# Kernel optimization log

Measured on AMD Instinct MI355X. Metric: run time of the kernel, lower is better.

Reference implementation:

```python
import jax, jax.numpy as jnp
import numpy as np

IN_DIM = 128
NUM_IDX = 128
LATENT = 512
FF_HID = 4 * IN_DIM
EPS = 1e-5


def _layernorm(x, g, b):
    mu = jnp.mean(x, axis=-1, keepdims=True)
    var = jnp.mean((x - mu) ** 2, axis=-1, keepdims=True)
    return (x - mu) * jax.lax.rsqrt(var + EPS) * g + b


def setup_inputs() -> dict:
    key = jax.random.key(0)
    ks = jax.random.split(key, 12)
    B, N, D, L = 16, NUM_IDX, IN_DIM, LATENT
    s = lambda fan_in: 1.0 / np.sqrt(fan_in)
    return {
        "in_obs": jax.random.normal(ks[0], (B, N, D), jnp.float32),
        "Wq_w": jax.random.normal(ks[1], (D, L), jnp.float32) * s(D),
        "Wq_b": jax.random.normal(ks[2], (L,), jnp.float32) * s(D),
        "Wk_w": jax.random.normal(ks[3], (D, L), jnp.float32) * s(D),
        "Wk_b": jax.random.normal(ks[4], (L,), jnp.float32) * s(D),
        "wv_w": jax.random.normal(ks[5], (2 * L + 2 * N,), jnp.float32) * s(2 * L + 2 * N),
        "wv_b": jax.random.normal(ks[6], (), jnp.float32) * s(2 * L + 2 * N),
        "g1": jnp.ones((D,), jnp.float32),
        "b1": jnp.zeros((D,), jnp.float32),
        "ff1_w": jax.random.normal(ks[7], (D, FF_HID), jnp.float32) * s(D),
        "ff1_b": jax.random.normal(ks[8], (FF_HID,), jnp.float32) * s(D),
        "ff2_w": jax.random.normal(ks[9], (FF_HID, D), jnp.float32) * s(FF_HID),
        "ff2_b": jax.random.normal(ks[10], (D,), jnp.float32) * s(FF_HID),
        "g2": jnp.ones((D,), jnp.float32),
        "b2": jnp.zeros((D,), jnp.float32),
    }


def reference(in_obs, Wq_w, Wq_b, Wk_w, Wk_b, wv_w, wv_b, g1, b1,
              ff1_w, ff1_b, ff2_w, ff2_b, g2, b2):
    # in_obs: [B, N, D]
    B, N, D = in_obs.shape
    L = Wq_w.shape[1]
    eye = jnp.broadcast_to(jnp.eye(N, dtype=in_obs.dtype), (B, N, N))
    # q_cat/k_cat: [B, N, L+N]
    q_cat = jnp.concatenate([in_obs @ Wq_w + Wq_b, eye], axis=-1)
    k_cat = jnp.concatenate([in_obs @ Wk_w + Wk_b, eye], axis=-1)
    # Original: w_v(tanh(concat(q_i, k_j))). tanh is elementwise and the dot
    # product splits over the concat, so score[b,i,j] = a[b,i] + c[b,j] + bias
    # -- mathematically identical, avoids the [B,N,N,2L+2N] intermediate.
    a = jnp.tanh(q_cat) @ wv_w[: L + N]          # [B, N]
    c = jnp.tanh(k_cat) @ wv_w[L + N:]           # [B, N]
    scores = a[:, :, None] + c[:, None, :] + wv_b  # [B, N, N]
    weights = jax.nn.softmax(scores, axis=-1)
    attn = weights @ in_obs                       # [B, N, D]
    res = _layernorm(attn + in_obs, g1, b1)
    ff = jax.nn.relu(res @ ff1_w + ff1_b) @ ff2_w + ff2_b
    return _layernorm(ff + in_obs, g2, b2)
```

## Files before the change

### kernel.cpp

```cpp
#include <hip/hip_runtime.h>

#define NN 128
#define DD 128
#define LL 512
#define FFH 512
#define TANH1 0.76159415595576489f

typedef __attribute__((ext_vector_type(8))) short bf16x8;
typedef __attribute__((ext_vector_type(4))) float f32x4;

struct alignas(16) f4arr { float v[4]; };

__device__ __forceinline__ unsigned short f2bf(float f) {
    union { float f; unsigned u; } v; v.f = f;
    return (unsigned short)((v.u + 0x7FFFu + ((v.u >> 16) & 1u)) >> 16);
}

__global__ __launch_bounds__(256) void kA(
    const float* __restrict__ in_obs,
    const float* __restrict__ Wk_w,
    const float* __restrict__ Wk_b,
    const float* __restrict__ wv_w,
    const float* __restrict__ ff1_w,
    const float* __restrict__ ff2_w,
    float* __restrict__ c_out,
    unsigned short* __restrict__ W1f,
    unsigned short* __restrict__ W2f)
{
    const int t = threadIdx.x;
    const int wave = t >> 6, lane = t & 63;
    __shared__ float row_lds[8][128];
    __shared__ float red[8][4];

    if (blockIdx.x >= 256) {
        const int bi = blockIdx.x - 256;
        const int l15 = lane & 15, l4 = lane >> 4;
        const int fg = (bi & 31) * 4 + wave;
        unsigned short vals[8];
        unsigned short* dst;
        if (bi < 32) {
            const int ks = fg & 3, mt = fg >> 2;
            #pragma unroll
            for (int j = 0; j < 8; ++j)
                vals[j] = f2bf(ff1_w[(ks * 32 + l4 * 8 + j) * FFH + mt * 16 + l15]);
            dst = W1f;
        } else {
            const int ks = fg & 15, mt = fg >> 4;
            #pragma unroll
            for (int j = 0; j < 8; ++j)
                vals[j] = f2bf(ff2_w[(ks * 32 + l4 * 8 + j) * DD + mt * 16 + l15]);
            dst = W2f;
        }
        uint4 u;
        u.x = (unsigned)vals[0] | ((unsigned)vals[1] << 16);
        u.y = (unsigned)vals[2] | ((unsigned)vals[3] << 16);
        u.z = (unsigned)vals[4] | ((unsigned)vals[5] << 16);
        u.w = (unsigned)vals[6] | ((unsigned)vals[7] << 16);
        *(uint4*)&dst[(fg * 64 + lane) * 8] = u;
        return;
    }

    const int row0 = blockIdx.x * 8;
    const float* src = in_obs + row0 * DD;
    #pragma unroll
    for (int i = 0; i < 4; ++i) {
        int idx = t + i * 256;
        row_lds[idx >> 7][idx & 127] = src[idx];
    }
    __syncthreads();

    const int l0 = t, l1 = t + 256;
    float acc0[8], acc1[8];
    #pragma unroll
    for (int r = 0; r < 8; ++r) { acc0[r] = 0.f; acc1[r] = 0.f; }

    #pragma unroll 4
    for (int d = 0; d < 128; d += 4) {
        f4arr rbuf[8];
        #pragma unroll
        for (int r = 0; r < 8; ++r)
            rbuf[r] = *(const f4arr*)&row_lds[r][d];
        #pragma unroll
        for (int dd = 0; dd < 4; ++dd) {
            const float w0 = Wk_w[(d + dd) * LL + l0];
            const float w1 = Wk_w[(d + dd) * LL + l1];
            #pragma unroll
            for (int r = 0; r < 8; ++r) {
                acc0[r] += rbuf[r].v[dd] * w0;
                acc1[r] += rbuf[r].v[dd] * w1;
            }
        }
    }
    const float kb0 = Wk_b[l0], kb1 = Wk_b[l1];
    const float wv0 = wv_w[640 + l0], wv1 = wv_w[640 + l1];
    float v[8];
    #pragma unroll
    for (int r = 0; r < 8; ++r)
        v[r] = tanhf(acc0[r] + kb0) * wv0 + tanhf(acc1[r] + kb1) * wv1;
    #pragma unroll
    for (int off = 32; off > 0; off >>= 1) {
        #pragma unroll
        for (int r = 0; r < 8; ++r)
            v[r] += __shfl_down(v[r], off, 64);
    }
    if (lane == 0) {
        #pragma unroll
        for (int r = 0; r < 8; ++r) red[r][wave] = v[r];
    }
    __syncthreads();
    if (t < 8) {
        const int row = row0 + t;
        const int j = row & (NN - 1);
        c_out[row] = red[t][0] + red[t][1] + red[t][2] + red[t][3]
                   + TANH1 * wv_w[1152 + j];
    }
}

__global__ __launch_bounds__(512, 4) void kB(
    const float* __restrict__ in_obs,
    const float* __restrict__ c_in,
    const unsigned short* __restrict__ W1f,
    const unsigned short* __restrict__ W2f,
    const float* __restrict__ g1, const float* __restrict__ b1,
    const float* __restrict__ ff1_b,
    const float* __restrict__ ff2_b,
    const float* __restrict__ g2, const float* __restrict__ b2,
    float* __restrict__ out)
{
    const int t = threadIdx.x;
    const int b = blockIdx.x >> 5;
    const int j0 = (blockIdx.x & 31) * 4;
    const int wave = t >> 6, lane = t & 63;
    const int l15 = lane & 15, l4 = lane >> 4;

    __shared__ float part[8][128];
    __shared__ alignas(16) unsigned short res_lds[16 * 128];
    __shared__ alignas(16) unsigned short h_lds[16 * 512];
    __shared__ alignas(16) float o2_lds[16 * 128];

    const float cv0 = c_in[b * NN + lane];
    const float cv1 = c_in[b * NN + lane + 64];
    float mx = fmaxf(cv0, cv1);
    #pragma unroll
    for (int off = 32; off > 0; off >>= 1) mx = fmaxf(mx, __shfl_xor(mx, off, 64));
    float e0 = __expf(cv0 - mx), e1 = __expf(cv1 - mx);
    float sm = e0 + e1;
    #pragma unroll
    for (int off = 32; off > 0; off >>= 1) sm += __shfl_xor(sm, off, 64);
    const float inv = 1.f / sm;
    e0 *= inv; e1 *= inv;

    {
        const float* base = in_obs + (b * NN + wave * 16) * DD;
        float a0 = 0.f, a1 = 0.f;
        #pragma unroll
        for (int jj = 0; jj < 16; ++jj) {
            const int js = wave * 16 + jj;
            const float wj = (wave < 4) ? __shfl(e0, js, 64)
                                        : __shfl(e1, js - 64, 64);
            a0 += wj * base[jj * DD + lane];
            a1 += wj * base[jj * DD + 64 + lane];
        }
        part[wave][lane] = a0;
        part[wave][lane + 64] = a1;
    }
    __syncthreads();

    if (wave < 4) {
        const int r = wave;
        const int row = b * NN + j0 + r;
        const int c0i = lane * 2;
        const float2 xo = *(const float2*)&in_obs[row * DD + c0i];
        float x0 = xo.x, x1 = xo.y;
        #pragma unroll
        for (int g = 0; g < 8; ++g) {
            const float2 p = *(const float2*)&part[g][c0i];
            x0 += p.x; x1 += p.y;
        }
        float s = x0 + x1;
        #pragma unroll
        for (int off = 32; off > 0; off >>= 1) s += __shfl_xor(s, off, 64);
        const float mu = s * (1.f / 128.f);
        const float d0 = x0 - mu, d1 = x1 - mu;
        float vs = d0 * d0 + d1 * d1;
        #pragma unroll
        for (int off = 32; off > 0; off >>= 1) vs += __shfl_xor(vs, off, 64);
        const float rstd = rsqrtf(vs * (1.f / 128.f) + 1e-5f);
        const float2 gv = *(const float2*)&g1[c0i];
        const float2 bv = *(const float2*)&b1[c0i];
        const float r0 = d0 * rstd * gv.x + bv.x;
        const float r1 = d1 * rstd * gv.y + bv.y;
        const unsigned pk = (unsigned)f2bf(r0) | ((unsigned)f2bf(r1) << 16);
        const int swz = (lane * 4) ^ ((r & 7) << 4);
        *(unsigned*)((char*)res_lds + r * 256 + swz) = pk;
    } else {
        #pragma unroll
        for (int k = 0; k < 3; ++k) {
            const int r = wave + k * 4;
            *(unsigned*)((char*)res_lds + r * 256 + lane * 4) = 0u;
        }
    }
    __syncthreads();

    {
        bf16x8 bfrag[4];
        #pragma unroll
        for (int ks = 0; ks < 4; ++ks) {
            const int off = l15 * 256 + ((ks * 64 + l4 * 16) ^ ((l15 & 7) << 4));
            bfrag[ks] = *(const bf16x8*)((const char*)res_lds + off);
        }
        #pragma unroll
        for (int i = 0; i < 4; ++i) {
            const int mt = wave * 4 + i;
            f32x4 acc = {0.f, 0.f, 0.f, 0.f};
            #pragma unroll
            for (int ks = 0; ks < 4; ++ks) {
                const bf16x8 afrag = *(const bf16x8*)(W1f + ((mt * 4 + ks) * 64 + lane) * 8);
                acc = __builtin_amdgcn_mfma_f32_16x16x32_bf16(afrag, bfrag[ks], acc, 0, 0, 0);
            }
            const f4arr bias = *(const f4arr*)&ff1_b[mt * 16 + l4 * 4];
            uint2 pk;
            pk.x = (unsigned)f2bf(fmaxf(acc[0] + bias.v[0], 0.f))
                 | ((unsigned)f2bf(fmaxf(acc[1] + bias.v[1], 0.f)) << 16);
            pk.y = (unsigned)f2bf(fmaxf(acc[2] + bias.v[2], 0.f))
                 | ((unsigned)f2bf(fmaxf(acc[3] + bias.v[3], 0.f)) << 16);
            const int off = l15 * 1024 + ((mt * 32 + l4 * 8) ^ ((l15 & 7) << 4));
            *(uint2*)((char*)h_lds + off) = pk;
        }
    }
    __syncthreads();

    {
        f32x4 acc = {0.f, 0.f, 0.f, 0.f};
        #pragma unroll
        for (int ks = 0; ks < 16; ++ks) {
            const int off = l15 * 1024 + ((ks * 64 + l4 * 16) ^ ((l15 & 7) << 4));
            const bf16x8 bfrag = *(const bf16x8*)((const char*)h_lds + off);
            const bf16x8 afrag = *(const bf16x8*)(W2f + ((wave * 16 + ks) * 64 + lane) * 8);
            acc = __builtin_amdgcn_mfma_f32_16x16x32_bf16(afrag, bfrag, acc, 0, 0, 0);
        }
        const int off = l15 * 512 + ((wave * 64 + l4 * 16) ^ ((l15 & 7) << 4));
        *(f32x4*)((char*)o2_lds + off) = acc;
    }
    __syncthreads();

    if (wave < 4) {
        const int r = wave;
        const int row = b * NN + j0 + r;
        const int c0i = lane * 2;
        const int off = r * 512 + ((lane * 8) ^ ((r & 7) << 4));
        const float2 o2 = *(const float2*)((char*)o2_lds + off);
        const float2 fb = *(const float2*)&ff2_b[c0i];
        const float2 xo = *(const float2*)&in_obs[row * DD + c0i];
        const float f0 = o2.x + fb.x + xo.x;
        const float f1 = o2.y + fb.y + xo.y;
        float s = f0 + f1;
        #pragma unroll
        for (int off2 = 32; off2 > 0; off2 >>= 1) s += __shfl_xor(s, off2, 64);
        const float mu = s * (1.f / 128.f);
        const float d0 = f0 - mu, d1 = f1 - mu;
        float vs = d0 * d0 + d1 * d1;
        #pragma unroll
        for (int off2 = 32; off2 > 0; off2 >>= 1) vs += __shfl_xor(vs, off2, 64);
        const float rstd = rsqrtf(vs * (1.f / 128.f) + 1e-5f);
        const float2 gv = *(const float2*)&g2[c0i];
        const float2 bv = *(const float2*)&b2[c0i];
        float2 o;
        o.x = d0 * rstd * gv.x + bv.x;
        o.y = d1 * rstd * gv.y + bv.y;
        *(float2*)&out[row * DD + c0i] = o;
    }
}

extern "C" void kernel_launch(void* const* d_in, const int* in_sizes, int n_in,
                              void* d_out, int out_size, void* d_ws, size_t ws_size,
                              hipStream_t stream) {
    const float* in_obs = (const float*)d_in[0];
    const float* Wk_w  = (const float*)d_in[3];
    const float* Wk_b  = (const float*)d_in[4];
    const float* wv_w  = (const float*)d_in[5];
    const float* g1    = (const float*)d_in[7];
    const float* b1    = (const float*)d_in[8];
    const float* ff1_w = (const float*)d_in[9];
    const float* ff1_b = (const float*)d_in[10];
    const float* ff2_w = (const float*)d_in[11];
    const float* ff2_b = (const float*)d_in[12];
    const float* g2    = (const float*)d_in[13];
    const float* b2    = (const float*)d_in[14];
    float* outp = (float*)d_out;

    unsigned short* W1f = (unsigned short*)d_ws;
    unsigned short* W2f = W1f + 65536;
    float* c_ws = (float*)((char*)d_ws + 262144);

    kA<<<320, 256, 0, stream>>>(in_obs, Wk_w, Wk_b, wv_w, ff1_w, ff2_w,
                                c_ws, W1f, W2f);
    kB<<<512, 512, 0, stream>>>(in_obs, c_ws, W1f, W2f, g1, b1,
                                ff1_b, ff2_b, g2, b2, outp);
}
```

Measured before the change: 28.17 us.

## Fill all 16 MFMA rows per block in kB and spread weight conversion across more blocks

kB now handles 16 output rows per block instead of 4, so the 16-wide MFMA tile is fully used instead of 12 rows being zero padding. This cuts the grid from 512 to 128 blocks, which removes repeated per-block work: the batch softmax/attention reduction and the full W1f/W2f weight reads. In kA, the bf16 weight-fragment conversion is spread over 256 blocks, each thread packing two values, instead of 64 blocks doing eight values per thread. The trade-off is that 128 kB blocks may leave many CUs idle, and each wave now runs two layernorm rows in sequence.

```diff
diff --git a/kernel.cpp b/kernel.cpp
--- a/kernel.cpp
+++ b/kernel.cpp
@@ -29,37 +29,32 @@
 {
     const int t = threadIdx.x;
     const int wave = t >> 6, lane = t & 63;
-    __shared__ float row_lds[8][128];
-    __shared__ float red[8][4];
 
     if (blockIdx.x >= 256) {
         const int bi = blockIdx.x - 256;
+        const int fg = bi & 127;
+        const int jp = t >> 6;
         const int l15 = lane & 15, l4 = lane >> 4;
-        const int fg = (bi & 31) * 4 + wave;
-        unsigned short vals[8];
+        const int j = jp * 2;
+        unsigned short v0, v1;
         unsigned short* dst;
-        if (bi < 32) {
+        if (bi < 128) {
             const int ks = fg & 3, mt = fg >> 2;
-            #pragma unroll
-            for (int j = 0; j < 8; ++j)
-                vals[j] = f2bf(ff1_w[(ks * 32 + l4 * 8 + j) * FFH + mt * 16 + l15]);
+            v0 = f2bf(ff1_w[(ks * 32 + l4 * 8 + j    ) * FFH + mt * 16 + l15]);
+            v1 = f2bf(ff1_w[(ks * 32 + l4 * 8 + j + 1) * FFH + mt * 16 + l15]);
             dst = W1f;
         } else {
             const int ks = fg & 15, mt = fg >> 4;
-            #pragma unroll
-            for (int j = 0; j < 8; ++j)
-                vals[j] = f2bf(ff2_w[(ks * 32 + l4 * 8 + j) * DD + mt * 16 + l15]);
+            v0 = f2bf(ff2_w[(ks * 32 + l4 * 8 + j    ) * DD + mt * 16 + l15]);
+            v1 = f2bf(ff2_w[(ks * 32 + l4 * 8 + j + 1) * DD + mt * 16 + l15]);
             dst = W2f;
         }
-        uint4 u;
-        u.x = (unsigned)vals[0] | ((unsigned)vals[1] << 16);
-        u.y = (unsigned)vals[2] | ((unsigned)vals[3] << 16);
-        u.z = (unsigned)vals[4] | ((unsigned)vals[5] << 16);
-        u.w = (unsigned)vals[6] | ((unsigned)vals[7] << 16);
-        *(uint4*)&dst[(fg * 64 + lane) * 8] = u;
+        *(unsigned*)&dst[(fg * 64 + lane) * 8 + j] = (unsigned)v0 | ((unsigned)v1 << 16);
         return;
     }
 
+    __shared__ float row_lds[8][128];
+    __shared__ float red[8][4];
     const int row0 = blockIdx.x * 8;
     const float* src = in_obs + row0 * DD;
     #pragma unroll
@@ -128,8 +123,8 @@
     float* __restrict__ out)
 {
     const int t = threadIdx.x;
-    const int b = blockIdx.x >> 5;
-    const int j0 = (blockIdx.x & 31) * 4;
+    const int b = blockIdx.x >> 3;
+    const int j0 = (blockIdx.x & 7) * 16;
     const int wave = t >> 6, lane = t & 63;
     const int l15 = lane & 15, l4 = lane >> 4;
 
@@ -166,38 +161,36 @@
     }
     __syncthreads();
 
-    if (wave < 4) {
-        const int r = wave;
-        const int row = b * NN + j0 + r;
+    {
         const int c0i = lane * 2;
-        const float2 xo = *(const float2*)&in_obs[row * DD + c0i];
-        float x0 = xo.x, x1 = xo.y;
+        float a0 = 0.f, a1 = 0.f;
         #pragma unroll
         for (int g = 0; g < 8; ++g) {
             const float2 p = *(const float2*)&part[g][c0i];
-            x0 += p.x; x1 += p.y;
-        }
-        float s = x0 + x1;
-        #pragma unroll
-        for (int off = 32; off > 0; off >>= 1) s += __shfl_xor(s, off, 64);
-        const float mu = s * (1.f / 128.f);
-        const float d0 = x0 - mu, d1 = x1 - mu;
-        float vs = d0 * d0 + d1 * d1;
-        #pragma unroll
-        for (int off = 32; off > 0; off >>= 1) vs += __shfl_xor(vs, off, 64);
-        const float rstd = rsqrtf(vs * (1.f / 128.f) + 1e-5f);
+            a0 += p.x; a1 += p.y;
+        }
         const float2 gv = *(const float2*)&g1[c0i];
         const float2 bv = *(const float2*)&b1[c0i];
-        const float r0 = d0 * rstd * gv.x + bv.x;
-        const float r1 = d1 * rstd * gv.y + bv.y;
-        const unsigned pk = (unsigned)f2bf(r0) | ((unsigned)f2bf(r1) << 16);
-        const int swz = (lane * 4) ^ ((r & 7) << 4);
-        *(unsigned*)((char*)res_lds + r * 256 + swz) = pk;
-    } else {
-        #pragma unroll
-        for (int k = 0; k < 3; ++k) {
-            const int r = wave + k * 4;
-            *(unsigned*)((char*)res_lds + r * 256 + lane * 4) = 0u;
+        #pragma unroll
+        for (int rr = 0; rr < 2; ++rr) {
+            const int r = wave + rr * 8;
+            const int row = b * NN + j0 + r;
+            const float2 xo = *(const float2*)&in_obs[row * DD + c0i];
+            const float x0 = a0 + xo.x, x1 = a1 + xo.y;
+            float s = x0 + x1;
+            #pragma unroll
+            for (int off = 32; off > 0; off >>= 1) s += __shfl_xor(s, off, 64);
+            const float mu = s * (1.f / 128.f);
+            const float d0 = x0 - mu, d1 = x1 - mu;
+            float vs = d0 * d0 + d1 * d1;
+            #pragma unroll
+            for (int off = 32; off > 0; off >>= 1) vs += __shfl_xor(vs, off, 64);
+            const float rstd = rsqrtf(vs * (1.f / 128.f) + 1e-5f);
+            const float r0 = d0 * rstd * gv.x + bv.x;
+            const float r1 = d1 * rstd * gv.y + bv.y;
+            const unsigned pk = (unsigned)f2bf(r0) | ((unsigned)f2bf(r1) << 16);
+            const int swz = (lane * 4) ^ ((r & 7) << 4);
+            *(unsigned*)((char*)res_lds + r * 256 + swz) = pk;
         }
     }
     __syncthreads();
@@ -244,31 +237,34 @@
     }
     __syncthreads();
 
-    if (wave < 4) {
-        const int r = wave;
-        const int row = b * NN + j0 + r;
+    {
         const int c0i = lane * 2;
-        const int off = r * 512 + ((lane * 8) ^ ((r & 7) << 4));
-        const float2 o2 = *(const float2*)((char*)o2_lds + off);
         const float2 fb = *(const float2*)&ff2_b[c0i];
-        const float2 xo = *(const float2*)&in_obs[row * DD + c0i];
-        const float f0 = o2.x + fb.x + xo.x;
-        const float f1 = o2.y + fb.y + xo.y;
-        float s = f0 + f1;
-        #pragma unroll
-        for (int off2 = 32; off2 > 0; off2 >>= 1) s += __shfl_xor(s, off2, 64);
-        const float mu = s * (1.f / 128.f);
-        const float d0 = f0 - mu, d1 = f1 - mu;
-        float vs = d0 * d0 + d1 * d1;
-        #pragma unroll
-        for (int off2 = 32; off2 > 0; off2 >>= 1) vs += __shfl_xor(vs, off2, 64);
-        const float rstd = rsqrtf(vs * (1.f / 128.f) + 1e-5f);
         const float2 gv = *(const float2*)&g2[c0i];
         const float2 bv = *(const float2*)&b2[c0i];
-        float2 o;
-        o.x = d0 * rstd * gv.x + bv.x;
-        o.y = d1 * rstd * gv.y + bv.y;
-        *(float2*)&out[row * DD + c0i] = o;
+        #pragma unroll
+        for (int rr = 0; rr < 2; ++rr) {
+            const int r = wave + rr * 8;
+            const int row = b * NN + j0 + r;
+            const int off = r * 512 + ((lane * 8) ^ ((r & 7) << 4));
+            const float2 o2 = *(const float2*)((char*)o2_lds + off);
+            const float2 xo = *(const float2*)&in_obs[row * DD + c0i];
+            const float f0 = o2.x + fb.x + xo.x;
+            const float f1 = o2.y + fb.y + xo.y;
+            float s = f0 + f1;
+            #pragma unroll
+            for (int off2 = 32; off2 > 0; off2 >>= 1) s += __shfl_xor(s, off2, 64);
+            const float mu = s * (1.f / 128.f);
+            const float d0 = f0 - mu, d1 = f1 - mu;
+            float vs = d0 * d0 + d1 * d1;
+            #pragma unroll
+            for (int off2 = 32; off2 > 0; off2 >>= 1) vs += __shfl_xor(vs, off2, 64);
+            const float rstd = rsqrtf(vs * (1.f / 128.f) + 1e-5f);
+            float2 o;
+            o.x = d0 * rstd * gv.x + bv.x;
+            o.y = d1 * rstd * gv.y + bv.y;
+            *(float2*)&out[row * DD + c0i] = o;
+        }
     }
 }
 
@@ -293,8 +289,8 @@
     unsigned short* W2f = W1f + 65536;
     float* c_ws = (float*)((char*)d_ws + 262144);
 
-    kA<<<320, 256, 0, stream>>>(in_obs, Wk_w, Wk_b, wv_w, ff1_w, ff2_w,
+    kA<<<512, 256, 0, stream>>>(in_obs, Wk_w, Wk_b, wv_w, ff1_w, ff2_w,
                                 c_ws, W1f, W2f);
-    kB<<<512, 512, 0, stream>>>(in_obs, c_ws, W1f, W2f, g1, b1,
+    kB<<<128, 512, 0, stream>>>(in_obs, c_ws, W1f, W2f, g1, b1,
                                 ff1_b, ff2_b, g2, b2, outp);
 }
```

Measured after the change: 26.17 us. -7.1%, faster.

## Replicate bf16 FFN weight fragments eight times across XCDs for kB reads

Applied to the files above, without the earlier changes.

The weight pre-pack in kA now writes eight copies of the bf16 fragment-ordered ff1/ff2 weights, one per value of blockIdx&7, using 256 extra blocks that each pack 8 fragment groups with 2 elements per thread. kB picks its copy by blk&7, so blocks on the same XCD (round-robin dispatch) read the same copy and hit their local L2. The aim is to cut cross-XCD traffic and contention on a single weight buffer. In exchange it uses 8x the workspace, makes kA write 8x more bytes with narrower 4-byte stores, and adds 256 blocks to kA.

```diff
diff --git a/kernel.cpp b/kernel.cpp
--- a/kernel.cpp
+++ b/kernel.cpp
@@ -5,6 +5,7 @@
 #define LL 512
 #define FFH 512
 #define TANH1 0.76159415595576489f
+#define CPY 65536
 
 typedef __attribute__((ext_vector_type(8))) short bf16x8;
 typedef __attribute__((ext_vector_type(4))) float f32x4;
@@ -28,39 +29,41 @@
     unsigned short* __restrict__ W2f)
 {
     const int t = threadIdx.x;
+    const int blk = blockIdx.x;
     const int wave = t >> 6, lane = t & 63;
+
+    if (blk >= 256) {
+        const int x = blk & 7;
+        const int s = (blk - 256) >> 3;
+        const int jp = t >> 6;
+        const int pl = t & 63;
+        const int pl15 = pl & 15, pl4 = pl >> 4;
+        const int j = jp * 2;
+        #pragma unroll
+        for (int f = 0; f < 8; ++f) {
+            const int fg = s * 8 + f;
+            unsigned short v0, v1;
+            unsigned short* dst;
+            if (fg < 128) {
+                const int ks = fg & 3, mt = fg >> 2;
+                v0 = f2bf(ff1_w[(ks * 32 + pl4 * 8 + j    ) * FFH + mt * 16 + pl15]);
+                v1 = f2bf(ff1_w[(ks * 32 + pl4 * 8 + j + 1) * FFH + mt * 16 + pl15]);
+                dst = W1f + x * CPY + (fg * 64 + pl) * 8 + j;
+            } else {
+                const int fgw = fg - 128;
+                const int ks = fgw & 15, mt = fgw >> 4;
+                v0 = f2bf(ff2_w[(ks * 32 + pl4 * 8 + j    ) * DD + mt * 16 + pl15]);
+                v1 = f2bf(ff2_w[(ks * 32 + pl4 * 8 + j + 1) * DD + mt * 16 + pl15]);
+                dst = W2f + x * CPY + (fgw * 64 + pl) * 8 + j;
+            }
+            *(unsigned*)dst = (unsigned)v0 | ((unsigned)v1 << 16);
+        }
+        return;
+    }
+
     __shared__ float row_lds[8][128];
     __shared__ float red[8][4];
-
-    if (blockIdx.x >= 256) {
-        const int bi = blockIdx.x - 256;
-        const int l15 = lane & 15, l4 = lane >> 4;
-        const int fg = (bi & 31) * 4 + wave;
-        unsigned short vals[8];
-        unsigned short* dst;
-        if (bi < 32) {
-            const int ks = fg & 3, mt = fg >> 2;
-            #pragma unroll
-            for (int j = 0; j < 8; ++j)
-                vals[j] = f2bf(ff1_w[(ks * 32 + l4 * 8 + j) * FFH + mt * 16 + l15]);
-            dst = W1f;
-        } else {
-            const int ks = fg & 15, mt = fg >> 4;
-            #pragma unroll
-            for (int j = 0; j < 8; ++j)
-                vals[j] = f2bf(ff2_w[(ks * 32 + l4 * 8 + j) * DD + mt * 16 + l15]);
-            dst = W2f;
-        }
-        uint4 u;
-        u.x = (unsigned)vals[0] | ((unsigned)vals[1] << 16);
-        u.y = (unsigned)vals[2] | ((unsigned)vals[3] << 16);
-        u.z = (unsigned)vals[4] | ((unsigned)vals[5] << 16);
-        u.w = (unsigned)vals[6] | ((unsigned)vals[7] << 16);
-        *(uint4*)&dst[(fg * 64 + lane) * 8] = u;
-        return;
-    }
-
-    const int row0 = blockIdx.x * 8;
+    const int row0 = blk * 8;
     const float* src = in_obs + row0 * DD;
     #pragma unroll
     for (int i = 0; i < 4; ++i) {
@@ -128,10 +131,13 @@
     float* __restrict__ out)
 {
     const int t = threadIdx.x;
-    const int b = blockIdx.x >> 5;
-    const int j0 = (blockIdx.x & 31) * 4;
+    const int blk = blockIdx.x;
+    const int b = blk >> 5;
+    const int j0 = (blk & 31) * 4;
     const int wave = t >> 6, lane = t & 63;
     const int l15 = lane & 15, l4 = lane >> 4;
+    const unsigned short* W1x = W1f + (blk & 7) * CPY;
+    const unsigned short* W2x = W2f + (blk & 7) * CPY;
 
     __shared__ float part[8][128];
     __shared__ alignas(16) unsigned short res_lds[16 * 128];
@@ -215,7 +221,7 @@
             f32x4 acc = {0.f, 0.f, 0.f, 0.f};
             #pragma unroll
             for (int ks = 0; ks < 4; ++ks) {
-                const bf16x8 afrag = *(const bf16x8*)(W1f + ((mt * 4 + ks) * 64 + lane) * 8);
+                const bf16x8 afrag = *(const bf16x8*)(W1x + ((mt * 4 + ks) * 64 + lane) * 8);
                 acc = __builtin_amdgcn_mfma_f32_16x16x32_bf16(afrag, bfrag[ks], acc, 0, 0, 0);
             }
             const f4arr bias = *(const f4arr*)&ff1_b[mt * 16 + l4 * 4];
@@ -236,7 +242,7 @@
         for (int ks = 0; ks < 16; ++ks) {
             const int off = l15 * 1024 + ((ks * 64 + l4 * 16) ^ ((l15 & 7) << 4));
             const bf16x8 bfrag = *(const bf16x8*)((const char*)h_lds + off);
-            const bf16x8 afrag = *(const bf16x8*)(W2f + ((wave * 16 + ks) * 64 + lane) * 8);
+            const bf16x8 afrag = *(const bf16x8*)(W2x + ((wave * 16 + ks) * 64 + lane) * 8);
             acc = __builtin_amdgcn_mfma_f32_16x16x32_bf16(afrag, bfrag, acc, 0, 0, 0);
         }
         const int off = l15 * 512 + ((wave * 64 + l4 * 16) ^ ((l15 & 7) << 4));
@@ -290,10 +296,10 @@
     float* outp = (float*)d_out;
 
     unsigned short* W1f = (unsigned short*)d_ws;
-    unsigned short* W2f = W1f + 65536;
-    float* c_ws = (float*)((char*)d_ws + 262144);
-
-    kA<<<320, 256, 0, stream>>>(in_obs, Wk_w, Wk_b, wv_w, ff1_w, ff2_w,
+    unsigned short* W2f = W1f + 8 * CPY;
+    float* c_ws = (float*)((char*)d_ws + 2097152);
+
+    kA<<<512, 256, 0, stream>>>(in_obs, Wk_w, Wk_b, wv_w, ff1_w, ff2_w,
                                 c_ws, W1f, W2f);
     kB<<<512, 512, 0, stream>>>(in_obs, c_ws, W1f, W2f, g1, b1,
                                 ff1_b, ff2_b, g2, b2, outp);
```

Result: no change. 27.84 us (-1.2%).
